# Kernel optimization log

Hardware: AMD Instinct MI355X
Metric: run time of the kernel (lower is better)

Reference implementation:

```python
import jax, jax.numpy as jnp
import numpy as np
import math

B, L, D, H = 2, 2048, 1024, 16

def setup_inputs() -> dict:
    key = jax.random.key(0)
    ks = jax.random.split(key, 5)
    return {
        "query": jax.random.normal(ks[0], (B, L, D), dtype=jnp.float32),
        "key": jax.random.normal(ks[1], (B, L, D), dtype=jnp.float32),
        "value": jax.random.normal(ks[2], (B, L, D), dtype=jnp.float32),
        "w_out": jax.random.normal(ks[3], (D, D), dtype=jnp.float32) * (1.0 / math.sqrt(D)),
        "b_out": jnp.zeros((D,), dtype=jnp.float32),
    }

def reference(query, key, value, w_out, b_out):
    b, l, d_model = query.shape
    num_heads = H
    head_dim = d_model // num_heads
    scaling = 1.0 / math.sqrt(d_model)  # NOTE: module scales by embed_dim, not head_dim

    def reshape(x):
        return x.reshape(b, l, num_heads, head_dim).transpose(0, 2, 1, 3)  # [B,H,L,hd]

    q, k, v = reshape(query), reshape(key), reshape(value)
    scores = jnp.einsum("bhqd,bhkd->bhqk", q, k) * scaling  # [B,H,L,L]

    u = max(1, int(math.ceil(math.log(l + 1))))  # static: 8 for L=2048
    _, topk_idx = jax.lax.top_k(scores, u)  # [B,H,L,u]

    # scatter True at top-u key positions per query
    bi = jnp.arange(b)[:, None, None, None]
    hi = jnp.arange(num_heads)[None, :, None, None]
    qi = jnp.arange(l)[None, None, :, None]
    mask = jnp.zeros(scores.shape, dtype=bool).at[bi, hi, qi, topk_idx].set(True)

    scores_masked = jnp.where(mask, scores, -jnp.inf)
    attn_weights = jax.nn.softmax(scores_masked, axis=-1)  # [B,H,L,L]

    attn_out = jnp.einsum("bhqk,bhkd->bhqd", attn_weights, v)
    attn_out = attn_out.transpose(0, 2, 1, 3).reshape(b, l, d_model)
    attn_out = attn_out @ w_out.T + b_out  # nn.Linear
    return attn_out, attn_weights
```

## Files before the change

kernel.cpp:

```cpp
#include <hip/hip_runtime.h>
#include <math.h>

#define BB 2
#define LL 2048
#define DD 1024
#define HH 16
#define SCALE 0.03125f

#define ATTN_ELEMS ((size_t)BB * LL * DD)

typedef unsigned short u16;
typedef __attribute__((ext_vector_type(8))) short bf16x8;
typedef __attribute__((ext_vector_type(4))) short s16x4;
typedef __attribute__((ext_vector_type(4))) float f32x4;

__device__ __forceinline__ u16 f2bf_rne(float f) {
    union { float f; unsigned u; } c; c.f = f;
    unsigned u = c.u;
    u += 0x7fffu + ((u >> 16) & 1u);
    return (u16)(u >> 16);
}

__device__ __forceinline__ void splitbf(float x, short& h, short& l) {
    union { float f; unsigned u; } c; c.f = x;
    unsigned uh = c.u & 0xFFFF0000u;
    h = (short)(uh >> 16);
    union { unsigned u; float f; } ch; ch.u = uh;
    l = (short)f2bf_rne(x - ch.f);
}

__device__ __forceinline__ void insert8(float (&tv)[8], int (&ti)[8], float cv, int ci) {
    bool g0 = cv > tv[0], g1 = cv > tv[1], g2 = cv > tv[2], g3 = cv > tv[3],
         g4 = cv > tv[4], g5 = cv > tv[5], g6 = cv > tv[6];
    tv[7] = g6 ? tv[6] : cv;                 ti[7] = g6 ? ti[6] : ci;
    tv[6] = g5 ? tv[5] : (g6 ? cv : tv[6]);  ti[6] = g5 ? ti[5] : (g6 ? ci : ti[6]);
    tv[5] = g4 ? tv[4] : (g5 ? cv : tv[5]);  ti[5] = g4 ? ti[4] : (g5 ? ci : ti[5]);
    tv[4] = g3 ? tv[3] : (g4 ? cv : tv[4]);  ti[4] = g3 ? ti[3] : (g4 ? ci : ti[4]);
    tv[3] = g2 ? tv[2] : (g3 ? cv : tv[3]);  ti[3] = g2 ? ti[2] : (g3 ? ci : ti[3]);
    tv[2] = g1 ? tv[1] : (g2 ? cv : tv[2]);  ti[2] = g1 ? ti[1] : (g2 ? ci : ti[2]);
    tv[1] = g0 ? tv[0] : (g1 ? cv : tv[1]);  ti[1] = g0 ? ti[0] : (g1 ? ci : ti[1]);
    tv[0] = g0 ? cv : tv[0];                 ti[0] = g0 ? ci : ti[0];
}

__device__ __forceinline__ void merge4(
    const float* v0, const int* i0, const float* v1, const int* i1,
    const float* v2, const int* i2, const float* v3, const int* i3,
    float* ov, int* oi)
{
    int p0 = 0, p1 = 0, p2 = 0, p3 = 0;
    #pragma unroll
    for (int s = 0; s < 8; ++s) {
        float a0 = v0[p0], a1 = v1[p1], a2 = v2[p2], a3 = v3[p3];
        int   b0 = i0[p0], b1 = i1[p1], b2 = i2[p2], b3 = i3[p3];
        float bv = a0; int bi = b0; int bc = 0;
        if (a1 > bv || (a1 == bv && b1 < bi)) { bv = a1; bi = b1; bc = 1; }
        if (a2 > bv || (a2 == bv && b2 < bi)) { bv = a2; bi = b2; bc = 2; }
        if (a3 > bv || (a3 == bv && b3 < bi)) { bv = a3; bi = b3; bc = 3; }
        p0 += (bc == 0); p1 += (bc == 1); p2 += (bc == 2); p3 += (bc == 3);
        ov[s] = bv; oi[s] = bi;
    }
}


__global__ __launch_bounds__(256) void prep_k_kernel(
    const float* __restrict__ k, u16* __restrict__ khi, u16* __restrict__ klo)
{
    int gid = blockIdx.x * 256 + threadIdx.x;
    int li   = gid & 15;
    int qd   = (gid >> 4) & 3;
    int c    = (gid >> 6) & 1;
    int s    = (gid >> 7) & 127;
    int head = gid >> 14;
    int b = head >> 4, h = head & 15;
    const float* src = k + ((size_t)(b * LL + s * 16 + li)) * DD + h * 64 + c * 32 + qd * 8;
    float x[8];
    *(f32x4*)x       = *(const f32x4*)src;
    *(f32x4*)(x + 4) = *(const f32x4*)(src + 4);
    bf16x8 h8, l8;
    #pragma unroll
    for (int e = 0; e < 8; ++e) { short hh, ll; splitbf(x[e], hh, ll); h8[e] = hh; l8[e] = ll; }
    *(bf16x8*)&khi[(size_t)gid * 8] = h8;
    *(bf16x8*)&klo[(size_t)gid * 8] = l8;
}

__global__ __launch_bounds__(256) void prep_w_kernel(
    const float* __restrict__ w, u16* __restrict__ whi, u16* __restrict__ wlo)
{
    int gid = blockIdx.x * 256 + threadIdx.x;
    int li = gid & 15;
    int qd = (gid >> 4) & 3;
    int c  = (gid >> 6) & 3;
    int nt = (gid >> 8) & 3;
    int kc = (gid >> 10) & 7;
    int nb = gid >> 13;
    const float* src = w + (size_t)(nb * 64 + nt * 16 + li) * DD + kc * 128 + c * 32 + qd * 8;
    float x[8];
    *(f32x4*)x       = *(const f32x4*)src;
    *(f32x4*)(x + 4) = *(const f32x4*)(src + 4);
    bf16x8 h8, l8;
    #pragma unroll
    for (int e = 0; e < 8; ++e) { short hh, ll; splitbf(x[e], hh, ll); h8[e] = hh; l8[e] = ll; }
    *(bf16x8*)&whi[(size_t)gid * 8] = h8;
    *(bf16x8*)&wlo[(size_t)gid * 8] = l8;
}

__global__ __launch_bounds__(256) void attn_fast_kernel(
    const float* __restrict__ q, const float* __restrict__ k, const float* __restrict__ v,
    const u16* __restrict__ khi_g, const u16* __restrict__ klo_g,
    float* __restrict__ aw, u16* __restrict__ chi, u16* __restrict__ clo)
{
    const int bid  = blockIdx.x;
    const int qt   = bid & 31;
    const int h    = (bid >> 5) & 15;
    const int b    = bid >> 9;
    const int t    = threadIdx.x;
    const int wv   = t >> 6;
    const int lane = t & 63;
    const int li   = lane & 15;
    const int quad = lane >> 4;

    __shared__ float mv[4096];
    __shared__ int   mi[4096];
    __shared__ float s2v[32][4][8];
    __shared__ int   s2i[32][4][8];
    __shared__ int   cidx[32][12];
    __shared__ float cs[32][12];
    __shared__ float wrow[64][8];
    __shared__ int   wix[64][8];

    f32x4* awz = (f32x4*)(aw + (((size_t)(b * HH + h) * LL) + (size_t)qt * 64) * LL);
    const f32x4 zero4 = {0.f, 0.f, 0.f, 0.f};

    bf16x8 qh0, ql0, qh1, ql1;
    {
        const float* qrow = q + ((size_t)(b * LL + qt * 64 + wv * 16 + li)) * DD + h * 64;
        float x[8];
        *(f32x4*)x       = *(const f32x4*)(qrow + quad * 8);
        *(f32x4*)(x + 4) = *(const f32x4*)(qrow + quad * 8 + 4);
        #pragma unroll
        for (int e = 0; e < 8; ++e) { short hh, ll; splitbf(x[e], hh, ll); qh0[e] = hh; ql0[e] = ll; }
        *(f32x4*)x       = *(const f32x4*)(qrow + 32 + quad * 8);
        *(f32x4*)(x + 4) = *(const f32x4*)(qrow + 32 + quad * 8 + 4);
        #pragma unroll
        for (int e = 0; e < 8; ++e) { short hh, ll; splitbf(x[e], hh, ll); qh1[e] = hh; ql1[e] = ll; }
    }

    float tv[4][8]; int tix[4][8];
    #pragma unroll
    for (int r = 0; r < 4; ++r)
        #pragma unroll
        for (int s = 0; s < 8; ++s) { tv[r][s] = -INFINITY; tix[r][s] = 0; }

    const u16* khb = khi_g + (size_t)(b * HH + h) * 131072 + (size_t)lane * 8;
    const u16* klb = klo_g + (size_t)(b * HH + h) * 131072 + (size_t)lane * 8;

    bf16x8 kh0 = *(const bf16x8*)(khb);
    bf16x8 kh1 = *(const bf16x8*)(khb + 512);
    bf16x8 kl0 = *(const bf16x8*)(klb);
    bf16x8 kl1 = *(const bf16x8*)(klb + 512);

    #pragma unroll 2
    for (int s = 0; s < 128; ++s) {
        const int sn = (s + 1) & 127;
        bf16x8 nh0 = *(const bf16x8*)(khb + (size_t)sn * 1024);
        bf16x8 nh1 = *(const bf16x8*)(khb + (size_t)sn * 1024 + 512);
        bf16x8 nl0 = *(const bf16x8*)(klb + (size_t)sn * 1024);
        bf16x8 nl1 = *(const bf16x8*)(klb + (size_t)sn * 1024 + 512);

        awz[s * 256 + t] = zero4;

        f32x4 c4a = {0.f, 0.f, 0.f, 0.f};
        f32x4 c4b = {0.f, 0.f, 0.f, 0.f};
        c4a = __builtin_amdgcn_mfma_f32_16x16x32_bf16(qh0, kh0, c4a, 0, 0, 0);
        c4b = __builtin_amdgcn_mfma_f32_16x16x32_bf16(qh1, kh1, c4b, 0, 0, 0);
        c4a = __builtin_amdgcn_mfma_f32_16x16x32_bf16(qh0, kl0, c4a, 0, 0, 0);
        c4b = __builtin_amdgcn_mfma_f32_16x16x32_bf16(qh1, kl1, c4b, 0, 0, 0);
        c4a = __builtin_amdgcn_mfma_f32_16x16x32_bf16(ql0, kh0, c4a, 0, 0, 0);
        c4b = __builtin_amdgcn_mfma_f32_16x16x32_bf16(ql1, kh1, c4b, 0, 0, 0);

        int ci = s * 16 + li;
        #pragma unroll
        for (int r = 0; r < 4; ++r) {
            float cv = (c4a[r] + c4b[r]) * SCALE;
            if (cv > tv[r][7]) insert8(tv[r], tix[r], cv, ci);
        }
        kh0 = nh0; kh1 = nh1; kl0 = nl0; kl1 = nl1;
    }

    for (int bb = 0; bb < 2; ++bb) {
        __syncthreads();
        if ((wv >> 1) == bb) {
            int rl0 = (wv & 1) * 16 + quad * 4;
            #pragma unroll
            for (int r = 0; r < 4; ++r) {
                int base = (rl0 + r) * 128 + li * 8;
                #pragma unroll
                for (int s = 0; s < 8; ++s) { mv[base + s] = tv[r][s]; mi[base + s] = tix[r][s]; }
            }
        }
        __syncthreads();
        if (t < 128) {
            int rr = t >> 2, p = t & 3;
            int base = rr * 128 + p * 32;
            merge4(&mv[base], &mi[base], &mv[base + 8], &mi[base + 8],
                   &mv[base + 16], &mi[base + 16], &mv[base + 24], &mi[base + 24],
                   s2v[rr][p], s2i[rr][p]);
        }
        __syncthreads();
        if (t < 32) {
            int rr = t;
            int pp[4] = {0, 0, 0, 0};
            #pragma unroll
            for (int s = 0; s < 12; ++s) {
                float bv = -INFINITY; int bi = 0x7fffffff; int bc = 0;
                #pragma unroll
                for (int l = 0; l < 4; ++l) {
                    if (pp[l] < 8) {
                        float hv = s2v[rr][l][pp[l]]; int hi2 = s2i[rr][l][pp[l]];
                        if (hv > bv || (hv == bv && hi2 < bi)) { bv = hv; bi = hi2; bc = l; }
                    }
                }
                pp[bc] += 1;
                cidx[rr][s] = bi;
            }
        }
        __syncthreads();
        for (int task = t; task < 384; task += 256) {
            int row = task / 12, c = task - row * 12;
            const float* qp = q + ((size_t)(b * LL + qt * 64 + bb * 32 + row)) * DD + h * 64;
            const float* kp = k + ((size_t)(b * LL + cidx[row][c])) * DD + h * 64;
            float acc = 0.f;
            for (int d4 = 0; d4 < 16; ++d4) {
                f32x4 qa = *(const f32x4*)(qp + d4 * 4);
                f32x4 ka = *(const f32x4*)(kp + d4 * 4);
                acc = fmaf(qa[0], ka[0], acc);
                acc = fmaf(qa[1], ka[1], acc);
                acc = fmaf(qa[2], ka[2], acc);
                acc = fmaf(qa[3], ka[3], acc);
            }
            cs[row][c] = acc * SCALE;
        }
        __syncthreads();
        if (t < 32) {
            int rr = t;
            float vv[12]; int ii[12];
            #pragma unroll
            for (int c = 0; c < 12; ++c) { vv[c] = cs[rr][c]; ii[c] = cidx[rr][c]; }
            float fv[8]; int fi[8];
            #pragma unroll
            for (int s = 0; s < 8; ++s) {
                float bv = -INFINITY; int bi = 0x7fffffff; int bc = 0;
                #pragma unroll
                for (int c = 0; c < 12; ++c) {
                    if (vv[c] > bv || (vv[c] == bv && ii[c] < bi)) { bv = vv[c]; bi = ii[c]; bc = c; }
                }
                vv[bc] = -INFINITY;
                fv[s] = bv; fi[s] = bi;
            }
            float m = fv[0];
            float e0[8]; float sum = 0.f;
            #pragma unroll
            for (int s = 0; s < 8; ++s) { e0[s] = __expf(fv[s] - m); sum += e0[s]; }
            float inv = 1.0f / sum;
            int grow = bb * 32 + rr;
            float* awrow = aw + (((size_t)(b * HH + h) * LL) + (size_t)qt * 64 + grow) * LL;
            #pragma unroll
            for (int s = 0; s < 8; ++s) {
                float w8 = e0[s] * inv;
                awrow[fi[s]] = w8;
                wrow[grow][s] = w8; wix[grow][s] = fi[s];
            }
        }
    }
    __syncthreads();

    const float* vbase = v + ((size_t)b * LL) * DD + h * 64;
    #pragma unroll
    for (int i = 0; i < 4; ++i) {
        int id = i * 256 + t;
        int row = id >> 4, seg = id & 15;
        f32x4 acc = {0.f, 0.f, 0.f, 0.f};
        #pragma unroll
        for (int s = 0; s < 8; ++s) {
            float ws = wrow[row][s];
            f32x4 vvv = *(const f32x4*)(vbase + (size_t)wix[row][s] * DD + seg * 4);
            acc[0] = fmaf(ws, vvv[0], acc[0]);
            acc[1] = fmaf(ws, vvv[1], acc[1]);
            acc[2] = fmaf(ws, vvv[2], acc[2]);
            acc[3] = fmaf(ws, vvv[3], acc[3]);
        }
        size_t off = ((size_t)(b * LL + qt * 64 + row)) * DD + h * 64 + seg * 4;
        s16x4 h4, l4;
        #pragma unroll
        for (int j = 0; j < 4; ++j) { short hh, ll; splitbf(acc[j], hh, ll); h4[j] = hh; l4[j] = ll; }
        *(s16x4*)(chi + off) = h4;
        *(s16x4*)(clo + off) = l4;
    }
}

__global__ __launch_bounds__(256) void linear_fast_kernel(
    const u16* __restrict__ chi, const u16* __restrict__ clo,
    const u16* __restrict__ whi, const u16* __restrict__ wlo,
    const float* __restrict__ bias, float* __restrict__ out)
{
    const int bid  = blockIdx.x;
    const int nb   = bid & 15, mb = bid >> 4;
    const int t    = threadIdx.x;
    const int wv   = t >> 6;
    const int lane = t & 63;
    const int li   = lane & 15;
    const int quad = lane >> 4;

    f32x4 acc0 = {0.f,0.f,0.f,0.f}, acc1 = {0.f,0.f,0.f,0.f},
          acc2 = {0.f,0.f,0.f,0.f}, acc3 = {0.f,0.f,0.f,0.f};

    const u16* ah_row = chi + (size_t)(mb * 64 + wv * 16 + li) * DD + quad * 8;
    const u16* al_row = clo + (size_t)(mb * 64 + wv * 16 + li) * DD + quad * 8;
    const size_t wboff = (size_t)nb * 65536 + (size_t)lane * 8;

    for (int kc = 0; kc < 8; ++kc) {
        const u16* wb_h = whi + wboff + kc * 8192;
        const u16* wb_l = wlo + wboff + kc * 8192;
        #pragma unroll
        for (int c = 0; c < 4; ++c) {
            bf16x8 ah = *(const bf16x8*)(ah_row + kc * 128 + c * 32);
            bf16x8 al = *(const bf16x8*)(al_row + kc * 128 + c * 32);
            bf16x8 bh0 = *(const bf16x8*)(wb_h + c * 512);
            bf16x8 bl0 = *(const bf16x8*)(wb_l + c * 512);
            bf16x8 bh1 = *(const bf16x8*)(wb_h + 2048 + c * 512);
            bf16x8 bl1 = *(const bf16x8*)(wb_l + 2048 + c * 512);
            bf16x8 bh2 = *(const bf16x8*)(wb_h + 4096 + c * 512);
            bf16x8 bl2 = *(const bf16x8*)(wb_l + 4096 + c * 512);
            bf16x8 bh3 = *(const bf16x8*)(wb_h + 6144 + c * 512);
            bf16x8 bl3 = *(const bf16x8*)(wb_l + 6144 + c * 512);
            acc0 = __builtin_amdgcn_mfma_f32_16x16x32_bf16(ah, bh0, acc0, 0, 0, 0);
            acc0 = __builtin_amdgcn_mfma_f32_16x16x32_bf16(ah, bl0, acc0, 0, 0, 0);
            acc0 = __builtin_amdgcn_mfma_f32_16x16x32_bf16(al, bh0, acc0, 0, 0, 0);
            acc1 = __builtin_amdgcn_mfma_f32_16x16x32_bf16(ah, bh1, acc1, 0, 0, 0);
            acc1 = __builtin_amdgcn_mfma_f32_16x16x32_bf16(ah, bl1, acc1, 0, 0, 0);
            acc1 = __builtin_amdgcn_mfma_f32_16x16x32_bf16(al, bh1, acc1, 0, 0, 0);
            acc2 = __builtin_amdgcn_mfma_f32_16x16x32_bf16(ah, bh2, acc2, 0, 0, 0);
            acc2 = __builtin_amdgcn_mfma_f32_16x16x32_bf16(ah, bl2, acc2, 0, 0, 0);
            acc2 = __builtin_amdgcn_mfma_f32_16x16x32_bf16(al, bh2, acc2, 0, 0, 0);
            acc3 = __builtin_amdgcn_mfma_f32_16x16x32_bf16(ah, bh3, acc3, 0, 0, 0);
            acc3 = __builtin_amdgcn_mfma_f32_16x16x32_bf16(ah, bl3, acc3, 0, 0, 0);
            acc3 = __builtin_amdgcn_mfma_f32_16x16x32_bf16(al, bh3, acc3, 0, 0, 0);
        }
    }

    #pragma unroll
    for (int st = 0; st < 4; ++st) {
        f32x4 a = (st == 0) ? acc0 : (st == 1) ? acc1 : (st == 2) ? acc2 : acc3;
        int col = nb * 64 + st * 16 + li;
        float bb2 = bias[col];
        #pragma unroll
        for (int r = 0; r < 4; ++r)
            out[(size_t)(mb * 64 + wv * 16 + quad * 4 + r) * DD + col] = a[r] + bb2;
    }
}


__global__ __launch_bounds__(256) void attn_kernel(
    const float* __restrict__ q, const float* __restrict__ k, const float* __restrict__ v,
    float* __restrict__ aw, float* __restrict__ ctx)
{
    const int bid  = blockIdx.x;
    const int qt   = bid & 31;
    const int h    = (bid >> 5) & 15;
    const int b    = bid >> 9;
    const int t    = threadIdx.x;
    const int wv   = t >> 6;
    const int lane = t & 63;
    const int li   = lane & 15;
    const int quad = lane >> 4;

    __shared__ __align__(16) char smA[32768];
    __shared__ float s2v[32][4][8];
    __shared__ int   s2i[32][4][8];
    __shared__ int   cidx[32][12];
    __shared__ float cs[32][12];
    __shared__ float wrow[64][8];
    __shared__ int   wix[64][8];
    u16* khi = (u16*)smA;
    u16* klo = (u16*)(smA + 16384);

    const float* kbase = k + ((size_t)b * LL) * DD + h * 64;
    f32x4* awz = (f32x4*)(aw + (((size_t)(b * HH + h) * LL) + (size_t)qt * 64) * LL);
    const f32x4 zero4 = {0.f, 0.f, 0.f, 0.f};

    bf16x8 qh0, ql0, qh1, ql1;
    {
        const float* qrow = q + ((size_t)(b * LL + qt * 64 + wv * 16 + li)) * DD + h * 64;
        float x[8];
        *(f32x4*)x       = *(const f32x4*)(qrow + quad * 8);
        *(f32x4*)(x + 4) = *(const f32x4*)(qrow + quad * 8 + 4);
        #pragma unroll
        for (int e = 0; e < 8; ++e) { short hh, ll; splitbf(x[e], hh, ll); qh0[e] = hh; ql0[e] = ll; }
        *(f32x4*)x       = *(const f32x4*)(qrow + 32 + quad * 8);
        *(f32x4*)(x + 4) = *(const f32x4*)(qrow + 32 + quad * 8 + 4);
        #pragma unroll
        for (int e = 0; e < 8; ++e) { short hh, ll; splitbf(x[e], hh, ll); qh1[e] = hh; ql1[e] = ll; }
    }

    float tv[4][8]; int tix[4][8];
    #pragma unroll
    for (int r = 0; r < 4; ++r)
        #pragma unroll
        for (int s = 0; s < 8; ++s) { tv[r][s] = -INFINITY; tix[r][s] = 0; }

    for (int iter = 0; iter < 16; ++iter) {
        __syncthreads();
        #pragma unroll
        for (int j = 0; j < 4; ++j) {
            int f   = j * 256 + t;
            int col = f >> 3;
            int c   = (f >> 2) & 1;
            int qd  = f & 3;
            const float* src = kbase + (size_t)(iter * 128 + col) * DD + c * 32 + qd * 8;
            float x[8];
            *(f32x4*)x       = *(const f32x4*)src;
            *(f32x4*)(x + 4) = *(const f32x4*)(src + 4);
            bf16x8 h8, l8;
            #pragma unroll
            for (int e = 0; e < 8; ++e) { short hh, ll; splitbf(x[e], hh, ll); h8[e] = hh; l8[e] = ll; }
            int off = (((col >> 4) * 2 + c) << 9) + (qd << 7) + ((col & 15) << 3);
            *(bf16x8*)&khi[off] = h8;
            *(bf16x8*)&klo[off] = l8;
        }
        #pragma unroll
        for (int i = 0; i < 8; ++i) awz[iter * 2048 + i * 256 + t] = zero4;
        __syncthreads();

        #pragma unroll
        for (int s = 0; s < 8; ++s) {
            int fo = s << 10;
            bf16x8 kh0 = *(bf16x8*)&khi[fo + (lane << 3)];
            bf16x8 kh1 = *(bf16x8*)&khi[fo + 512 + (lane << 3)];
            bf16x8 kl0 = *(bf16x8*)&klo[fo + (lane << 3)];
            bf16x8 kl1 = *(bf16x8*)&klo[fo + 512 + (lane << 3)];
            f32x4 c4 = {0.f, 0.f, 0.f, 0.f};
            c4 = __builtin_amdgcn_mfma_f32_16x16x32_bf16(qh0, kh0, c4, 0, 0, 0);
            c4 = __builtin_amdgcn_mfma_f32_16x16x32_bf16(qh1, kh1, c4, 0, 0, 0);
            c4 = __builtin_amdgcn_mfma_f32_16x16x32_bf16(qh0, kl0, c4, 0, 0, 0);
            c4 = __builtin_amdgcn_mfma_f32_16x16x32_bf16(qh1, kl1, c4, 0, 0, 0);
            c4 = __builtin_amdgcn_mfma_f32_16x16x32_bf16(ql0, kh0, c4, 0, 0, 0);
            c4 = __builtin_amdgcn_mfma_f32_16x16x32_bf16(ql1, kh1, c4, 0, 0, 0);
            int ci = iter * 128 + s * 16 + li;
            #pragma unroll
            for (int r = 0; r < 4; ++r) {
                float cv = c4[r] * SCALE;
                if (cv > tv[r][7]) insert8(tv[r], tix[r], cv, ci);
            }
        }
    }

    float* mv = (float*)smA;
    int*   mi = (int*)(smA + 16384);
    for (int bb = 0; bb < 2; ++bb) {
        __syncthreads();
        if ((wv >> 1) == bb) {
            int rl0 = (wv & 1) * 16 + quad * 4;
            #pragma unroll
            for (int r = 0; r < 4; ++r) {
                int base = (rl0 + r) * 128 + li * 8;
                #pragma unroll
                for (int s = 0; s < 8; ++s) { mv[base + s] = tv[r][s]; mi[base + s] = tix[r][s]; }
            }
        }
        __syncthreads();
        if (t < 128) {
            int rr = t >> 2, p = t & 3;
            int base = rr * 128 + p * 32;
            merge4(&mv[base], &mi[base], &mv[base + 8], &mi[base + 8],
                   &mv[base + 16], &mi[base + 16], &mv[base + 24], &mi[base + 24],
                   s2v[rr][p], s2i[rr][p]);
        }
        __syncthreads();
        if (t < 32) {
            int rr = t;
            int pp[4] = {0, 0, 0, 0};
            #pragma unroll
            for (int s = 0; s < 12; ++s) {
                float bv = -INFINITY; int bi = 0x7fffffff; int bc = 0;
                #pragma unroll
                for (int l = 0; l < 4; ++l) {
                    if (pp[l] < 8) {
                        float hv = s2v[rr][l][pp[l]]; int hi2 = s2i[rr][l][pp[l]];
                        if (hv > bv || (hv == bv && hi2 < bi)) { bv = hv; bi = hi2; bc = l; }
                    }
                }
                pp[bc] += 1;
                cidx[rr][s] = bi;
            }
        }
        __syncthreads();
        for (int task = t; task < 384; task += 256) {
            int row = task / 12, c = task - row * 12;
            const float* qp = q + ((size_t)(b * LL + qt * 64 + bb * 32 + row)) * DD + h * 64;
            const float* kp = k + ((size_t)(b * LL + cidx[row][c])) * DD + h * 64;
            float acc = 0.f;
            for (int d4 = 0; d4 < 16; ++d4) {
                f32x4 qa = *(const f32x4*)(qp + d4 * 4);
                f32x4 ka = *(const f32x4*)(kp + d4 * 4);
                acc = fmaf(qa[0], ka[0], acc);
                acc = fmaf(qa[1], ka[1], acc);
                acc = fmaf(qa[2], ka[2], acc);
                acc = fmaf(qa[3], ka[3], acc);
            }
            cs[row][c] = acc * SCALE;
        }
        __syncthreads();
        if (t < 32) {
            int rr = t;
            float vv[12]; int ii[12];
            #pragma unroll
            for (int c = 0; c < 12; ++c) { vv[c] = cs[rr][c]; ii[c] = cidx[rr][c]; }
            float fv[8]; int fi[8];
            #pragma unroll
            for (int s = 0; s < 8; ++s) {
                float bv = -INFINITY; int bi = 0x7fffffff; int bc = 0;
                #pragma unroll
                for (int c = 0; c < 12; ++c) {
                    if (vv[c] > bv || (vv[c] == bv && ii[c] < bi)) { bv = vv[c]; bi = ii[c]; bc = c; }
                }
                vv[bc] = -INFINITY;
                fv[s] = bv; fi[s] = bi;
            }
            float m = fv[0];
            float e0[8]; float sum = 0.f;
            #pragma unroll
            for (int s = 0; s < 8; ++s) { e0[s] = __expf(fv[s] - m); sum += e0[s]; }
            float inv = 1.0f / sum;
            int grow = bb * 32 + rr;
            float* awrow = aw + (((size_t)(b * HH + h) * LL) + (size_t)qt * 64 + grow) * LL;
            #pragma unroll
            for (int s = 0; s < 8; ++s) {
                float w8 = e0[s] * inv;
                awrow[fi[s]] = w8;
                wrow[grow][s] = w8; wix[grow][s] = fi[s];
            }
        }
    }
    __syncthreads();

    const float* vbase = v + ((size_t)b * LL) * DD + h * 64;
    #pragma unroll
    for (int i = 0; i < 4; ++i) {
        int id = i * 256 + t;
        int row = id >> 4, seg = id & 15;
        f32x4 acc = {0.f, 0.f, 0.f, 0.f};
        #pragma unroll
        for (int s = 0; s < 8; ++s) {
            float ws = wrow[row][s];
            f32x4 vvv = *(const f32x4*)(vbase + (size_t)wix[row][s] * DD + seg * 4);
            acc[0] = fmaf(ws, vvv[0], acc[0]);
            acc[1] = fmaf(ws, vvv[1], acc[1]);
            acc[2] = fmaf(ws, vvv[2], acc[2]);
            acc[3] = fmaf(ws, vvv[3], acc[3]);
        }
        *(f32x4*)(ctx + ((size_t)(b * LL + qt * 64 + row)) * DD + h * 64 + seg * 4) = acc;
    }
}

__global__ __launch_bounds__(256) void linear_ws_kernel(
    const float* __restrict__ ctx, const float* __restrict__ w,
    const float* __restrict__ bias, float* __restrict__ out)
{
    const int bid  = blockIdx.x;
    const int nb   = bid & 15, mb = bid >> 4;
    const int t    = threadIdx.x;
    const int wv   = t >> 6;
    const int lane = t & 63;
    const int li   = lane & 15;
    const int quad = lane >> 4;

    __shared__ u16 bhi[8192], blo[8192];

    f32x4 acc0 = {0.f,0.f,0.f,0.f}, acc1 = {0.f,0.f,0.f,0.f},
          acc2 = {0.f,0.f,0.f,0.f}, acc3 = {0.f,0.f,0.f,0.f};
    const float* arow = ctx + (size_t)(mb * 64 + wv * 16 + li) * DD;

    for (int kc = 0; kc < 8; ++kc) {
        __syncthreads();
        #pragma unroll
        for (int j = 0; j < 4; ++j) {
            int f   = j * 256 + t;
            int col = f >> 4;
            int c   = (f >> 2) & 3;
            int qd  = f & 3;
            const float* src = w + (size_t)(nb * 64 + col) * DD + kc * 128 + c * 32 + qd * 8;
            float x[8];
            *(f32x4*)x       = *(const f32x4*)src;
            *(f32x4*)(x + 4) = *(const f32x4*)(src + 4);
            bf16x8 h8, l8;
            #pragma unroll
            for (int e = 0; e < 8; ++e) { short hh, ll; splitbf(x[e], hh, ll); h8[e] = hh; l8[e] = ll; }
            int off = (((col >> 4) * 4 + c) << 9) + (qd << 7) + ((col & 15) << 3);
            *(bf16x8*)&bhi[off] = h8;
            *(bf16x8*)&blo[off] = l8;
        }
        __syncthreads();

        bf16x8 ah[4], al[4];
        #pragma unroll
        for (int c = 0; c < 4; ++c) {
            float x[8];
            *(f32x4*)x       = *(const f32x4*)(arow + kc * 128 + c * 32 + quad * 8);
            *(f32x4*)(x + 4) = *(const f32x4*)(arow + kc * 128 + c * 32 + quad * 8 + 4);
            #pragma unroll
            for (int e = 0; e < 8; ++e) { short hh, ll; splitbf(x[e], hh, ll); ah[c][e] = hh; al[c][e] = ll; }
        }
        #pragma unroll
        for (int c = 0; c < 4; ++c) {
            bf16x8 bh0 = *(bf16x8*)&bhi[(( 0 + c) << 9) + (lane << 3)];
            bf16x8 bl0 = *(bf16x8*)&blo[(( 0 + c) << 9) + (lane << 3)];
            bf16x8 bh1 = *(bf16x8*)&bhi[(( 4 + c) << 9) + (lane << 3)];
            bf16x8 bl1 = *(bf16x8*)&blo[(( 4 + c) << 9) + (lane << 3)];
            bf16x8 bh2 = *(bf16x8*)&bhi[(( 8 + c) << 9) + (lane << 3)];
            bf16x8 bl2 = *(bf16x8*)&blo[(( 8 + c) << 9) + (lane << 3)];
            bf16x8 bh3 = *(bf16x8*)&bhi[((12 + c) << 9) + (lane << 3)];
            bf16x8 bl3 = *(bf16x8*)&blo[((12 + c) << 9) + (lane << 3)];
            acc0 = __builtin_amdgcn_mfma_f32_16x16x32_bf16(ah[c], bh0, acc0, 0, 0, 0);
            acc0 = __builtin_amdgcn_mfma_f32_16x16x32_bf16(ah[c], bl0, acc0, 0, 0, 0);
            acc0 = __builtin_amdgcn_mfma_f32_16x16x32_bf16(al[c], bh0, acc0, 0, 0, 0);
            acc1 = __builtin_amdgcn_mfma_f32_16x16x32_bf16(ah[c], bh1, acc1, 0, 0, 0);
            acc1 = __builtin_amdgcn_mfma_f32_16x16x32_bf16(ah[c], bl1, acc1, 0, 0, 0);
            acc1 = __builtin_amdgcn_mfma_f32_16x16x32_bf16(al[c], bh1, acc1, 0, 0, 0);
            acc2 = __builtin_amdgcn_mfma_f32_16x16x32_bf16(ah[c], bh2, acc2, 0, 0, 0);
            acc2 = __builtin_amdgcn_mfma_f32_16x16x32_bf16(ah[c], bl2, acc2, 0, 0, 0);
            acc2 = __builtin_amdgcn_mfma_f32_16x16x32_bf16(al[c], bh2, acc2, 0, 0, 0);
            acc3 = __builtin_amdgcn_mfma_f32_16x16x32_bf16(ah[c], bh3, acc3, 0, 0, 0);
            acc3 = __builtin_amdgcn_mfma_f32_16x16x32_bf16(ah[c], bl3, acc3, 0, 0, 0);
            acc3 = __builtin_amdgcn_mfma_f32_16x16x32_bf16(al[c], bh3, acc3, 0, 0, 0);
        }
    }

    #pragma unroll
    for (int st = 0; st < 4; ++st) {
        f32x4 a = (st == 0) ? acc0 : (st == 1) ? acc1 : (st == 2) ? acc2 : acc3;
        int col = nb * 64 + st * 16 + li;
        float bb2 = bias[col];
        #pragma unroll
        for (int r = 0; r < 4; ++r)
            out[(size_t)(mb * 64 + wv * 16 + quad * 4 + r) * DD + col] = a[r] + bb2;
    }
}

__global__ __launch_bounds__(256) void linear_inplace_kernel(
    float* io, const float* __restrict__ w, const float* __restrict__ bias)
{
    __shared__ u16 ahi[16384], alo[16384];
    const int t    = threadIdx.x;
    const int m0   = blockIdx.x * 16;
    const int wv   = t >> 6;
    const int lane = t & 63;
    const int li   = lane & 15;
    const int quad = lane >> 4;

    #pragma unroll
    for (int i = 0; i < 8; ++i) {
        int id  = i * 256 + t;
        int row = id >> 7;
        int c   = (id >> 2) & 31;
        int qd  = id & 3;
        const float* src = io + (size_t)(m0 + row) * DD + c * 32 + qd * 8;
        float x[8];
        *(f32x4*)x       = *(const f32x4*)src;
        *(f32x4*)(x + 4) = *(const f32x4*)(src + 4);
        bf16x8 h8, l8;
        #pragma unroll
        for (int e = 0; e < 8; ++e) { short hh, ll; splitbf(x[e], hh, ll); h8[e] = hh; l8[e] = ll; }
        int off = (c << 9) + (qd << 7) + (row << 3);
        *(bf16x8*)&ahi[off] = h8;
        *(bf16x8*)&alo[off] = l8;
    }
    __syncthreads();

    f32x4 acc[16];
    #pragma unroll
    for (int i = 0; i < 16; ++i) acc[i] = (f32x4){0.f, 0.f, 0.f, 0.f};

    for (int c = 0; c < 32; ++c) {
        bf16x8 ah = *(bf16x8*)&ahi[(c << 9) + (lane << 3)];
        bf16x8 al = *(bf16x8*)&alo[(c << 9) + (lane << 3)];
        #pragma unroll
        for (int sub = 0; sub < 16; ++sub) {
            int col = wv * 256 + sub * 16 + li;
            const float* src = w + (size_t)col * DD + c * 32 + quad * 8;
            float x[8];
            *(f32x4*)x       = *(const f32x4*)src;
            *(f32x4*)(x + 4) = *(const f32x4*)(src + 4);
            bf16x8 bh, bl;
            #pragma unroll
            for (int e = 0; e < 8; ++e) { short hh, ll; splitbf(x[e], hh, ll); bh[e] = hh; bl[e] = ll; }
            acc[sub] = __builtin_amdgcn_mfma_f32_16x16x32_bf16(ah, bh, acc[sub], 0, 0, 0);
            acc[sub] = __builtin_amdgcn_mfma_f32_16x16x32_bf16(ah, bl, acc[sub], 0, 0, 0);
            acc[sub] = __builtin_amdgcn_mfma_f32_16x16x32_bf16(al, bh, acc[sub], 0, 0, 0);
        }
    }

    #pragma unroll
    for (int sub = 0; sub < 16; ++sub) {
        int col = wv * 256 + sub * 16 + li;
        float bb2 = bias[col];
        #pragma unroll
        for (int r = 0; r < 4; ++r)
            io[(size_t)(m0 + quad * 4 + r) * DD + col] = acc[sub][r] + bb2;
    }
}

extern "C" void kernel_launch(void* const* d_in, const int* in_sizes, int n_in,
                              void* d_out, int out_size, void* d_ws, size_t ws_size,
                              hipStream_t stream) {
    const float* q    = (const float*)d_in[0];
    const float* k    = (const float*)d_in[1];
    const float* v    = (const float*)d_in[2];
    const float* w    = (const float*)d_in[3];
    const float* bias = (const float*)d_in[4];

    float* out = (float*)d_out;
    float* aw  = out + ATTN_ELEMS;

    const size_t CHI_ELE = ATTN_ELEMS;
    const size_t KSP_ELE = 4194304;
    const size_t WSP_ELE = 1048576;
    const size_t need_fast = (2 * CHI_ELE + 2 * KSP_ELE + 2 * WSP_ELE) * sizeof(u16);

    if (d_ws != nullptr && ws_size >= need_fast) {
        u16* chi = (u16*)d_ws;
        u16* clo = chi + CHI_ELE;
        u16* khi = clo + CHI_ELE;
        u16* klo = khi + KSP_ELE;
        u16* whi = klo + KSP_ELE;
        u16* wlo = whi + WSP_ELE;
        prep_k_kernel<<<2048, 256, 0, stream>>>(k, khi, klo);
        prep_w_kernel<<<512, 256, 0, stream>>>(w, whi, wlo);
        attn_fast_kernel<<<BB * HH * (LL / 64), 256, 0, stream>>>(q, k, v, khi, klo, aw, chi, clo);
        linear_fast_kernel<<<(BB * LL / 64) * (DD / 64), 256, 0, stream>>>(chi, clo, whi, wlo, bias, out);
    } else {
        const bool use_ws = (d_ws != nullptr) && (ws_size >= ATTN_ELEMS * sizeof(float));
        float* ctx = use_ws ? (float*)d_ws : out;
        attn_kernel<<<BB * HH * (LL / 64), 256, 0, stream>>>(q, k, v, aw, ctx);
        if (use_ws) {
            linear_ws_kernel<<<(BB * LL / 64) * (DD / 64), 256, 0, stream>>>(ctx, w, bias, out);
        } else {
            linear_inplace_kernel<<<BB * LL / 16, 256, 0, stream>>>(out, w, bias);
        }
    }
}
```

Measured before the change: 886.6 us.

## Transpose MFMA operands so each lane keeps one top-12 list per query row

```diff
diff --git a/kernel.cpp b/kernel.cpp
--- a/kernel.cpp
+++ b/kernel.cpp
@@ -40,6 +40,24 @@
     tv[2] = g1 ? tv[1] : (g2 ? cv : tv[2]);  ti[2] = g1 ? ti[1] : (g2 ? ci : ti[2]);
     tv[1] = g0 ? tv[0] : (g1 ? cv : tv[1]);  ti[1] = g0 ? ti[0] : (g1 ? ci : ti[1]);
     tv[0] = g0 ? cv : tv[0];                 ti[0] = g0 ? ci : ti[0];
+}
+
+__device__ __forceinline__ void insert12(float (&tv)[12], int (&ti)[12], float cv, int ci) {
+    bool g0 = cv > tv[0], g1 = cv > tv[1], g2 = cv > tv[2], g3 = cv > tv[3],
+         g4 = cv > tv[4], g5 = cv > tv[5], g6 = cv > tv[6], g7 = cv > tv[7],
+         g8 = cv > tv[8], g9 = cv > tv[9], g10 = cv > tv[10];
+    tv[11] = g10 ? tv[10] : cv;                 ti[11] = g10 ? ti[10] : ci;
+    tv[10] = g9 ? tv[9] : (g10 ? cv : tv[10]);  ti[10] = g9 ? ti[9] : (g10 ? ci : ti[10]);
+    tv[9]  = g8 ? tv[8] : (g9 ? cv : tv[9]);    ti[9]  = g8 ? ti[8] : (g9 ? ci : ti[9]);
+    tv[8]  = g7 ? tv[7] : (g8 ? cv : tv[8]);    ti[8]  = g7 ? ti[7] : (g8 ? ci : ti[8]);
+    tv[7]  = g6 ? tv[6] : (g7 ? cv : tv[7]);    ti[7]  = g6 ? ti[6] : (g7 ? ci : ti[7]);
+    tv[6]  = g5 ? tv[5] : (g6 ? cv : tv[6]);    ti[6]  = g5 ? ti[5] : (g6 ? ci : ti[6]);
+    tv[5]  = g4 ? tv[4] : (g5 ? cv : tv[5]);    ti[5]  = g4 ? ti[4] : (g5 ? ci : ti[5]);
+    tv[4]  = g3 ? tv[3] : (g4 ? cv : tv[4]);    ti[4]  = g3 ? ti[3] : (g4 ? ci : ti[4]);
+    tv[3]  = g2 ? tv[2] : (g3 ? cv : tv[3]);    ti[3]  = g2 ? ti[2] : (g3 ? ci : ti[3]);
+    tv[2]  = g1 ? tv[1] : (g2 ? cv : tv[2]);    ti[2]  = g1 ? ti[1] : (g2 ? ci : ti[2]);
+    tv[1]  = g0 ? tv[0] : (g1 ? cv : tv[1]);    ti[1]  = g0 ? ti[0] : (g1 ? ci : ti[1]);
+    tv[0]  = g0 ? cv : tv[0];                   ti[0]  = g0 ? ci : ti[0];
 }
 
 __device__ __forceinline__ void merge4(
@@ -109,24 +127,19 @@
     const u16* __restrict__ khi_g, const u16* __restrict__ klo_g,
     float* __restrict__ aw, u16* __restrict__ chi, u16* __restrict__ clo)
 {
-    const int bid  = blockIdx.x;
-    const int qt   = bid & 31;
-    const int h    = (bid >> 5) & 15;
-    const int b    = bid >> 9;
+    const int swz  = (blockIdx.x & 7) * 128 + (blockIdx.x >> 3);
+    const int qt   = swz & 31;
+    const int h    = (swz >> 5) & 15;
+    const int b    = swz >> 9;
     const int t    = threadIdx.x;
     const int wv   = t >> 6;
     const int lane = t & 63;
     const int li   = lane & 15;
     const int quad = lane >> 4;
 
-    __shared__ float mv[4096];
-    __shared__ int   mi[4096];
-    __shared__ float s2v[32][4][8];
-    __shared__ int   s2i[32][4][8];
-    __shared__ int   cidx[32][12];
-    __shared__ float cs[32][12];
-    __shared__ float wrow[64][8];
-    __shared__ int   wix[64][8];
+    __shared__ float dv[64][48];
+    __shared__ u16   di_s[64][48];
+    __shared__ u16   cidx[64][12];
 
     f32x4* awz = (f32x4*)(aw + (((size_t)(b * HH + h) * LL) + (size_t)qt * 64) * LL);
     const f32x4 zero4 = {0.f, 0.f, 0.f, 0.f};
@@ -145,11 +158,9 @@
         for (int e = 0; e < 8; ++e) { short hh, ll; splitbf(x[e], hh, ll); qh1[e] = hh; ql1[e] = ll; }
     }
 
-    float tv[4][8]; int tix[4][8];
-    #pragma unroll
-    for (int r = 0; r < 4; ++r)
-        #pragma unroll
-        for (int s = 0; s < 8; ++s) { tv[r][s] = -INFINITY; tix[r][s] = 0; }
+    float tv[12]; int tix[12];
+    #pragma unroll
+    for (int s = 0; s < 12; ++s) { tv[s] = -INFINITY; tix[s] = 0; }
 
     const u16* khb = khi_g + (size_t)(b * HH + h) * 131072 + (size_t)lane * 8;
     const u16* klb = klo_g + (size_t)(b * HH + h) * 131072 + (size_t)lane * 8;
@@ -171,105 +182,98 @@
 
         f32x4 c4a = {0.f, 0.f, 0.f, 0.f};
         f32x4 c4b = {0.f, 0.f, 0.f, 0.f};
-        c4a = __builtin_amdgcn_mfma_f32_16x16x32_bf16(qh0, kh0, c4a, 0, 0, 0);
-        c4b = __builtin_amdgcn_mfma_f32_16x16x32_bf16(qh1, kh1, c4b, 0, 0, 0);
-        c4a = __builtin_amdgcn_mfma_f32_16x16x32_bf16(qh0, kl0, c4a, 0, 0, 0);
-        c4b = __builtin_amdgcn_mfma_f32_16x16x32_bf16(qh1, kl1, c4b, 0, 0, 0);
-        c4a = __builtin_amdgcn_mfma_f32_16x16x32_bf16(ql0, kh0, c4a, 0, 0, 0);
-        c4b = __builtin_amdgcn_mfma_f32_16x16x32_bf16(ql1, kh1, c4b, 0, 0, 0);
-
-        int ci = s * 16 + li;
+        c4a = __builtin_amdgcn_mfma_f32_16x16x32_bf16(kh0, qh0, c4a, 0, 0, 0);
+        c4b = __builtin_amdgcn_mfma_f32_16x16x32_bf16(kh1, qh1, c4b, 0, 0, 0);
+        c4a = __builtin_amdgcn_mfma_f32_16x16x32_bf16(kl0, qh0, c4a, 0, 0, 0);
+        c4b = __builtin_amdgcn_mfma_f32_16x16x32_bf16(kl1, qh1, c4b, 0, 0, 0);
+        c4a = __builtin_amdgcn_mfma_f32_16x16x32_bf16(kh0, ql0, c4a, 0, 0, 0);
+        c4b = __builtin_amdgcn_mfma_f32_16x16x32_bf16(kh1, ql1, c4b, 0, 0, 0);
+
+        const int ci0 = s * 16 + quad * 4;
         #pragma unroll
         for (int r = 0; r < 4; ++r) {
             float cv = (c4a[r] + c4b[r]) * SCALE;
-            if (cv > tv[r][7]) insert8(tv[r], tix[r], cv, ci);
+            if (cv > tv[11]) insert12(tv, tix, cv, ci0 + r);
         }
         kh0 = nh0; kh1 = nh1; kl0 = nl0; kl1 = nl1;
     }
 
-    for (int bb = 0; bb < 2; ++bb) {
-        __syncthreads();
-        if ((wv >> 1) == bb) {
-            int rl0 = (wv & 1) * 16 + quad * 4;
-            #pragma unroll
-            for (int r = 0; r < 4; ++r) {
-                int base = (rl0 + r) * 128 + li * 8;
-                #pragma unroll
-                for (int s = 0; s < 8; ++s) { mv[base + s] = tv[r][s]; mi[base + s] = tix[r][s]; }
+    {
+        const int row = wv * 16 + li;
+        #pragma unroll
+        for (int s = 0; s < 12; ++s) {
+            dv[row][quad * 12 + s]   = tv[s];
+            di_s[row][quad * 12 + s] = (u16)tix[s];
+        }
+    }
+    __syncthreads();
+
+    if (t < 64) {
+        const float* v0 = &dv[t][0];   const u16* i0 = &di_s[t][0];
+        const float* v1 = &dv[t][12];  const u16* i1 = &di_s[t][12];
+        const float* v2 = &dv[t][24];  const u16* i2 = &di_s[t][24];
+        const float* v3 = &dv[t][36];  const u16* i3 = &di_s[t][36];
+        int p0 = 0, p1 = 0, p2 = 0, p3 = 0;
+        #pragma unroll
+        for (int s = 0; s < 12; ++s) {
+            float a0 = v0[p0], a1 = v1[p1], a2 = v2[p2], a3 = v3[p3];
+            int   b0 = i0[p0], b1 = i1[p1], b2 = i2[p2], b3 = i3[p3];
+            float bv = a0; int bi = b0; int bc = 0;
+            if (a1 > bv || (a1 == bv && b1 < bi)) { bv = a1; bi = b1; bc = 1; }
+            if (a2 > bv || (a2 == bv && b2 < bi)) { bv = a2; bi = b2; bc = 2; }
+            if (a3 > bv || (a3 == bv && b3 < bi)) { bv = a3; bi = b3; bc = 3; }
+            p0 += (bc == 0); p1 += (bc == 1); p2 += (bc == 2); p3 += (bc == 3);
+            cidx[t][s] = (u16)bi;
+        }
+    }
+    __syncthreads();
+
+    float* cs = &dv[0][0];
+    for (int task = t; task < 768; task += 256) {
+        int row = task / 12, c = task - row * 12;
+        const float* qp = q + ((size_t)(b * LL + qt * 64 + row)) * DD + h * 64;
+        const float* kp = k + ((size_t)(b * LL + (int)cidx[row][c])) * DD + h * 64;
+        float acc = 0.f;
+        for (int d4 = 0; d4 < 16; ++d4) {
+            f32x4 qa = *(const f32x4*)(qp + d4 * 4);
+            f32x4 ka = *(const f32x4*)(kp + d4 * 4);
+            acc = fmaf(qa[0], ka[0], acc);
+            acc = fmaf(qa[1], ka[1], acc);
+            acc = fmaf(qa[2], ka[2], acc);
+            acc = fmaf(qa[3], ka[3], acc);
+        }
+        cs[row * 12 + c] = acc * SCALE;
+    }
+    __syncthreads();
+
+    float* wrow = &dv[0][0] + 1024;
+    int*   wix  = (int*)&di_s[0][0];
+    if (t < 64) {
+        float vv[12]; int ii[12];
+        #pragma unroll
+        for (int c = 0; c < 12; ++c) { vv[c] = cs[t * 12 + c]; ii[c] = (int)cidx[t][c]; }
+        float fv[8]; int fi[8];
+        #pragma unroll
+        for (int s = 0; s < 8; ++s) {
+            float bv = -INFINITY; int bi = 0x7fffffff; int bc = 0;
+            #pragma unroll
+            for (int c = 0; c < 12; ++c) {
+                if (vv[c] > bv || (vv[c] == bv && ii[c] < bi)) { bv = vv[c]; bi = ii[c]; bc = c; }
             }
-        }
-        __syncthreads();
-        if (t < 128) {
-            int rr = t >> 2, p = t & 3;
-            int base = rr * 128 + p * 32;
-            merge4(&mv[base], &mi[base], &mv[base + 8], &mi[base + 8],
-                   &mv[base + 16], &mi[base + 16], &mv[base + 24], &mi[base + 24],
-                   s2v[rr][p], s2i[rr][p]);
-        }
-        __syncthreads();
-        if (t < 32) {
-            int rr = t;
-            int pp[4] = {0, 0, 0, 0};
-            #pragma unroll
-            for (int s = 0; s < 12; ++s) {
-                float bv = -INFINITY; int bi = 0x7fffffff; int bc = 0;
-                #pragma unroll
-                for (int l = 0; l < 4; ++l) {
-                    if (pp[l] < 8) {
-                        float hv = s2v[rr][l][pp[l]]; int hi2 = s2i[rr][l][pp[l]];
-                        if (hv > bv || (hv == bv && hi2 < bi)) { bv = hv; bi = hi2; bc = l; }
-                    }
-                }
-                pp[bc] += 1;
-                cidx[rr][s] = bi;
-            }
-        }
-        __syncthreads();
-        for (int task = t; task < 384; task += 256) {
-            int row = task / 12, c = task - row * 12;
-            const float* qp = q + ((size_t)(b * LL + qt * 64 + bb * 32 + row)) * DD + h * 64;
-            const float* kp = k + ((size_t)(b * LL + cidx[row][c])) * DD + h * 64;
-            float acc = 0.f;
-            for (int d4 = 0; d4 < 16; ++d4) {
-                f32x4 qa = *(const f32x4*)(qp + d4 * 4);
-                f32x4 ka = *(const f32x4*)(kp + d4 * 4);
-                acc = fmaf(qa[0], ka[0], acc);
-                acc = fmaf(qa[1], ka[1], acc);
-                acc = fmaf(qa[2], ka[2], acc);
-                acc = fmaf(qa[3], ka[3], acc);
-            }
-            cs[row][c] = acc * SCALE;
-        }
-        __syncthreads();
-        if (t < 32) {
-            int rr = t;
-            float vv[12]; int ii[12];
-            #pragma unroll
-            for (int c = 0; c < 12; ++c) { vv[c] = cs[rr][c]; ii[c] = cidx[rr][c]; }
-            float fv[8]; int fi[8];
-            #pragma unroll
-            for (int s = 0; s < 8; ++s) {
-                float bv = -INFINITY; int bi = 0x7fffffff; int bc = 0;
-                #pragma unroll
-                for (int c = 0; c < 12; ++c) {
-                    if (vv[c] > bv || (vv[c] == bv && ii[c] < bi)) { bv = vv[c]; bi = ii[c]; bc = c; }
-                }
-                vv[bc] = -INFINITY;
-                fv[s] = bv; fi[s] = bi;
-            }
-            float m = fv[0];
-            float e0[8]; float sum = 0.f;
-            #pragma unroll
-            for (int s = 0; s < 8; ++s) { e0[s] = __expf(fv[s] - m); sum += e0[s]; }
-            float inv = 1.0f / sum;
-            int grow = bb * 32 + rr;
-            float* awrow = aw + (((size_t)(b * HH + h) * LL) + (size_t)qt * 64 + grow) * LL;
-            #pragma unroll
-            for (int s = 0; s < 8; ++s) {
-                float w8 = e0[s] * inv;
-                awrow[fi[s]] = w8;
-                wrow[grow][s] = w8; wix[grow][s] = fi[s];
-            }
+            vv[bc] = -INFINITY;
+            fv[s] = bv; fi[s] = bi;
+        }
+        float m = fv[0];
+        float e0[8]; float sum = 0.f;
+        #pragma unroll
+        for (int s = 0; s < 8; ++s) { e0[s] = __expf(fv[s] - m); sum += e0[s]; }
+        float inv = 1.0f / sum;
+        float* awrow = aw + (((size_t)(b * HH + h) * LL) + (size_t)qt * 64 + t) * LL;
+        #pragma unroll
+        for (int s = 0; s < 8; ++s) {
+            float w8 = e0[s] * inv;
+            awrow[fi[s]] = w8;
+            wrow[t * 8 + s] = w8; wix[t * 8 + s] = fi[s];
         }
     }
     __syncthreads();
@@ -282,8 +286,8 @@
         f32x4 acc = {0.f, 0.f, 0.f, 0.f};
         #pragma unroll
         for (int s = 0; s < 8; ++s) {
-            float ws = wrow[row][s];
-            f32x4 vvv = *(const f32x4*)(vbase + (size_t)wix[row][s] * DD + seg * 4);
+            float ws = wrow[row * 8 + s];
+            f32x4 vvv = *(const f32x4*)(vbase + (size_t)wix[row * 8 + s] * DD + seg * 4);
             acc[0] = fmaf(ws, vvv[0], acc[0]);
             acc[1] = fmaf(ws, vvv[1], acc[1]);
             acc[2] = fmaf(ws, vvv[2], acc[2]);
```

Measured after the change: 1.077 ms. 1.21x slower.
